# Kernel tuning notes

Measured on AMD Instinct MI355X. Metric: run time of the kernel, lower is better.

## Reference

```python
import jax, jax.numpy as jnp
import numpy as np

B, K, DIN, D, NH, HD, FF = 16384, 64, 49, 16, 2, 8, 32
EPS = 1e-5


def _ln(x, g, b):
    m = jnp.mean(x, axis=-1, keepdims=True)
    v = jnp.mean((x - m) ** 2, axis=-1, keepdims=True)
    return (x - m) / jnp.sqrt(v + EPS) * g + b


def setup_inputs() -> dict:
    key = jax.random.key(0)
    ks = jax.random.split(key, 20)
    s = 0.05
    return {
        "x": jax.random.normal(ks[0], (B, K, DIN), dtype=jnp.float32),
        # torch Linear layout: weight is [out, in]
        "proj_w": jax.random.normal(ks[1], (D, DIN), dtype=jnp.float32) * s,
        "proj_b": jax.random.normal(ks[2], (D,), dtype=jnp.float32) * s,
        "pos": jax.random.normal(ks[3], (1, K, D), dtype=jnp.float32) * s,
        "in_proj_w": jax.random.normal(ks[4], (3 * D, D), dtype=jnp.float32) * s,
        "in_proj_b": jax.random.normal(ks[5], (3 * D,), dtype=jnp.float32) * s,
        "out_w": jax.random.normal(ks[6], (D, D), dtype=jnp.float32) * s,
        "out_b": jax.random.normal(ks[7], (D,), dtype=jnp.float32) * s,
        "ln1_g": jnp.ones((D,), dtype=jnp.float32),
        "ln1_b": jnp.zeros((D,), dtype=jnp.float32),
        "lin1_w": jax.random.normal(ks[8], (FF, D), dtype=jnp.float32) * s,
        "lin1_b": jax.random.normal(ks[9], (FF,), dtype=jnp.float32) * s,
        "lin2_w": jax.random.normal(ks[10], (D, FF), dtype=jnp.float32) * s,
        "lin2_b": jax.random.normal(ks[11], (D,), dtype=jnp.float32) * s,
        "ln2_g": jnp.ones((D,), dtype=jnp.float32),
        "ln2_b": jnp.zeros((D,), dtype=jnp.float32),
        "head_w": jax.random.normal(ks[12], (1, D), dtype=jnp.float32) * s,
        "head_b": jax.random.normal(ks[13], (1,), dtype=jnp.float32) * s,
    }


def reference(x, proj_w, proj_b, pos, in_proj_w, in_proj_b, out_w, out_b,
              ln1_g, ln1_b, lin1_w, lin1_b, lin2_w, lin2_b, ln2_g, ln2_b,
              head_w, head_b):
    # input projection + learned positional embedding
    h = jnp.einsum("bki,di->bkd", x, proj_w) + proj_b + pos  # [B,K,D]

    # --- self-attention (torch MultiheadAttention, post-norm encoder layer) ---
    qkv = jnp.einsum("bkd,ed->bke", h, in_proj_w) + in_proj_b  # [B,K,3D]
    q, k, v = jnp.split(qkv, 3, axis=-1)
    q = q.reshape(B, K, NH, HD)
    k = k.reshape(B, K, NH, HD)
    v = v.reshape(B, K, NH, HD)
    scores = jnp.einsum("bqhd,bkhd->bhqk", q, k) / jnp.sqrt(jnp.float32(HD))
    attn = jax.nn.softmax(scores, axis=-1)
    ctx = jnp.einsum("bhqk,bkhd->bqhd", attn, v).reshape(B, K, D)
    attn_out = jnp.einsum("bkd,od->bko", ctx, out_w) + out_b
    h = _ln(h + attn_out, ln1_g, ln1_b)

    # --- FFN (relu), post-norm ---
    ff = jnp.einsum("bkd,fd->bkf", h, lin1_w) + lin1_b
    ff = jax.nn.relu(ff)
    ff = jnp.einsum("bkf,df->bkd", ff, lin2_w) + lin2_b
    h = _ln(h + ff, ln2_g, ln2_b)

    # mean pool over sequence, then scalar head
    pooled = h.mean(axis=1)  # [B,D]
    out = jnp.einsum("bd,od->bo", pooled, head_w) + head_b
    return out.squeeze(-1)  # [B]
```

## Files before the change

### kernel.cpp

```cpp
#include <hip/hip_runtime.h>


#define SCALE 0.510069729f

#define KRS   24
#define VTB   1536
#define VTS   72
#define HRB   2688
#define HRS   40
#define RED   5248
#define SMTOT 5256

#define WS_HB   2304
#define WS_EP   3328

typedef __bf16 v8bf __attribute__((ext_vector_type(8)));
typedef float  v4f  __attribute__((ext_vector_type(4)));

#define LDS_ORDER() __asm__ volatile("" ::: "memory")

static __device__ __forceinline__ short f2bs(float f) {
    __bf16 h = (__bf16)f;
    return __builtin_bit_cast(short, h);
}
#define MFMA(a,b,c) __builtin_amdgcn_mfma_f32_16x16x32_bf16((a),(b),(c),0,0,0)

template<int IMM> static __device__ __forceinline__ float swz(float x) {
    return __builtin_bit_cast(float,
        __builtin_amdgcn_ds_swizzle(__builtin_bit_cast(int, x), IMM));
}

template<int CTRL> static __device__ __forceinline__ float dppadd(float v) {
    int t = __builtin_amdgcn_update_dpp(0, __builtin_bit_cast(int, v),
                                        CTRL, 0xF, 0xF, true);
    return v + __builtin_bit_cast(float, t);
}

static __device__ __forceinline__ void red16(v4f& v) {
    #pragma unroll
    for (int r = 0; r < 4; ++r) v[r] = dppadd<0xB1>(v[r]);
    #pragma unroll
    for (int r = 0; r < 4; ++r) v[r] = dppadd<0x4E>(v[r]);
    #pragma unroll
    for (int r = 0; r < 4; ++r) v[r] = dppadd<0x124>(v[r]);
    #pragma unroll
    for (int r = 0; r < 4; ++r) v[r] = dppadd<0x128>(v[r]);
}

__global__ __launch_bounds__(256)
void tx_prep(const float* __restrict__ proj_w, const float* __restrict__ proj_b,
             const float* __restrict__ pos,
             const float* __restrict__ in_proj_w, const float* __restrict__ in_proj_b,
             const float* __restrict__ out_w, const float* __restrict__ out_b,
             const float* __restrict__ ln1_g, const float* __restrict__ ln1_b,
             const float* __restrict__ lin1_w, const float* __restrict__ lin1_b,
             const float* __restrict__ lin2_w, const float* __restrict__ lin2_b,
             const float* __restrict__ ln2_g, const float* __restrict__ ln2_b,
             const float* __restrict__ head_w, float* __restrict__ ws)
{
    const int tid = threadIdx.x;
    const int wv = tid >> 6, lane = tid & 63;
    const int g = lane >> 4, c = lane & 15;
    v8bf* wf = (v8bf*)ws;
    v8bf F;
    if (wv == 0) {
        #pragma unroll
        for (int j = 0; j < 8; ++j) F[j] = (__bf16)proj_w[c*49 + g*8 + j];
        wf[0*64 + lane] = F;
        #pragma unroll
        for (int j = 0; j < 8; ++j) {
            int k = (g == 0) ? (32 + j) : (g == 1) ? (40 + j)
                  : (g == 2 && j == 7) ? 48 : -1;
            F[j] = (k >= 0) ? (__bf16)proj_w[c*49 + k] : (__bf16)0.f;
        }
        wf[1*64 + lane] = F;
        #pragma unroll
        for (int nt = 0; nt < 3; ++nt) {
            #pragma unroll
            for (int j = 0; j < 8; ++j) { int k = g*8 + j; F[j] = (k < 16) ? (__bf16)in_proj_w[(nt*16 + c)*16 + k] : (__bf16)0.f; }
            wf[(2 + nt)*64 + lane] = F;
        }
    } else if (wv == 1) {
        #pragma unroll
        for (int j = 0; j < 8; ++j) { int k = g*8 + j; F[j] = (k < 16) ? (__bf16)out_w[c*16 + k] : (__bf16)0.f; }
        wf[5*64 + lane] = F;
        #pragma unroll
        for (int nt = 0; nt < 2; ++nt) {
            #pragma unroll
            for (int j = 0; j < 8; ++j) { int k = g*8 + j; F[j] = (k < 16) ? (__bf16)lin1_w[(nt*16 + c)*16 + k] : (__bf16)0.f; }
            wf[(6 + nt)*64 + lane] = F;
        }
        #pragma unroll
        for (int j = 0; j < 8; ++j) F[j] = (__bf16)lin2_w[c*32 + g*8 + j];
        wf[8*64 + lane] = F;
        if (lane < 16) {
            float* ep = ws + WS_EP + lane*16;
            ep[0]  = in_proj_b[lane];
            ep[1]  = in_proj_b[16 + lane] * SCALE;
            ep[2]  = in_proj_b[32 + lane];
            ep[3]  = out_b[lane];
            ep[4]  = ln1_g[lane];
            ep[5]  = ln1_b[lane];
            ep[6]  = lin1_b[lane];
            ep[7]  = lin1_b[16 + lane];
            ep[8]  = lin2_b[lane];
            ep[9]  = ln2_g[lane];
            ep[10] = ln2_b[lane];
            ep[11] = head_w[lane];
            ep[12] = 0.f; ep[13] = 0.f; ep[14] = 0.f; ep[15] = 0.f;
        }
    } else {
        float* hb = ws + WS_HB;
        const int w0 = (wv - 2) * 2;
        #pragma unroll
        for (int i = 0; i < 2; ++i) {
            int ww = w0 + i;
            #pragma unroll
            for (int r = 0; r < 4; ++r)
                hb[ww*256 + lane*4 + r] = proj_b[c] + pos[(ww*16 + g*4 + r)*16 + c];
        }
    }
}

__global__ __launch_bounds__(256, 8)
void tx_main(const float* __restrict__ x, const float* __restrict__ ws,
             const float* __restrict__ head_b, float* __restrict__ out)
{
    __shared__ __align__(16) short sm[SMTOT];
    const int tid   = threadIdx.x;
    const int w     = tid >> 6;
    const int lane  = tid & 63;
    const int g     = lane >> 4;
    const int c     = lane & 15;
    const int b     = blockIdx.x;
    const int myrow = w*16 + c;
    const int tok0  = w*16 + g*4;
    const v8bf* wf  = (const v8bf*)ws;
    const float4* ep4 = (const float4*)(ws + WS_EP);

    v8bf zfrag;
    #pragma unroll
    for (int j = 0; j < 8; ++j) zfrag[j] = (__bf16)0.f;
    const v4f zacc = {0.f, 0.f, 0.f, 0.f};

    *(unsigned long long*)&sm[HRB + myrow*HRS + 16 + g*4] = 0ull;
    if (lane < 16) {
        float4 z4 = {0.f, 0.f, 0.f, 0.f};
        *(float4*)&sm[(w*16 + lane)*KRS + 16] = z4;
    }

    v4f hC;
    {
        const float* xr = x + (size_t)b * 3136 + myrow*49;
        int off1 = 32 + g*8; if (off1 > 41) off1 = 41;
        v8bf a0, a1;
        #pragma unroll
        for (int j = 0; j < 8; ++j) a0[j] = (__bf16)xr[g*8 + j];
        #pragma unroll
        for (int j = 0; j < 8; ++j) a1[j] = (__bf16)xr[off1 + j];
        v4f hb = ((const v4f*)(ws + WS_HB))[w*64 + lane];
        hC = MFMA(a0, wf[0*64 + lane], hb);
        hC = MFMA(a1, wf[1*64 + lane], hC);
        #pragma unroll
        for (int r = 0; r < 4; ++r) sm[HRB + (tok0 + r)*HRS + c] = f2bs(hC[r]);
    }
    LDS_ORDER();

    {
        v8bf a = *(const v8bf*)&sm[HRB + myrow*HRS + g*8];
        v4f qC = MFMA(a, wf[2*64 + lane], zacc);
        v4f kC = MFMA(a, wf[3*64 + lane], zacc);
        v4f vC = MFMA(a, wf[4*64 + lane], zacc);
        float4 e0 = ep4[c*4];
        const int vsl = VTB + c*VTS + 32*(w >> 1) + 8*g + 4*(w & 1);
        #pragma unroll
        for (int r = 0; r < 4; ++r) {
            int tok = tok0 + r;
            sm[HRB + tok*HRS + c] = f2bs(qC[r] + e0.x);
            sm[tok*KRS + c]       = f2bs(fmaf(kC[r], SCALE, e0.y));
            sm[vsl + r]           = f2bs(vC[r] + e0.z);
        }
    }
    __syncthreads();

    v4f ctxC0, ctxC1;
    {
        v8bf aq = *(const v8bf*)&sm[HRB + myrow*HRS + g*8];
        #pragma unroll
        for (int hh = 0; hh < 2; ++hh) {
            v8bf bq = (g == hh) ? aq : zfrag;
            v8bf plo, phi;
            {
                v8bf ak0 = *(const v8bf*)&sm[(0*16 + c)*KRS + g*8];
                v8bf ak1 = *(const v8bf*)&sm[(1*16 + c)*KRS + g*8];
                v4f s0 = MFMA(ak0, bq, zacc);
                v4f s1 = MFMA(ak1, bq, zacc);
                #pragma unroll
                for (int r = 0; r < 4; ++r) {
                    plo[r]     = (__bf16)__builtin_amdgcn_exp2f(s0[r]);
                    plo[4 + r] = (__bf16)__builtin_amdgcn_exp2f(s1[r]);
                }
                v8bf ak2 = *(const v8bf*)&sm[(2*16 + c)*KRS + g*8];
                v8bf ak3 = *(const v8bf*)&sm[(3*16 + c)*KRS + g*8];
                v4f s2 = MFMA(ak2, bq, zacc);
                v4f s3 = MFMA(ak3, bq, zacc);
                #pragma unroll
                for (int r = 0; r < 4; ++r) {
                    phi[r]     = (__bf16)__builtin_amdgcn_exp2f(s2[r]);
                    phi[4 + r] = (__bf16)__builtin_amdgcn_exp2f(s3[r]);
                }
            }
            v8bf bv0 = zfrag, bv1 = zfrag;
            bool act  = (hh == 0) ? (c < 8) : (c >= 8);
            int  onec = (hh == 0) ? 8 : 7;
            if (act) {
                bv0 = *(const v8bf*)&sm[VTB + c*VTS + g*8];
                bv1 = *(const v8bf*)&sm[VTB + c*VTS + 32 + g*8];
            } else if (c == onec) {
                #pragma unroll
                for (int j = 0; j < 8; ++j) { bv0[j] = (__bf16)1.f; bv1[j] = (__bf16)1.f; }
            }
            v4f acc = MFMA(plo, bv0, zacc);
            acc = MFMA(phi, bv1, acc);
            if (hh) ctxC1 = acc; else ctxC0 = acc;
        }
    }

    {
        #pragma unroll
        for (int r = 0; r < 4; ++r) {
            float l0 = swz<0x110>(ctxC0[r]);
            float l1 = swz<0x0F0>(ctxC1[r]);
            float num = (c < 8) ? ctxC0[r] : ctxC1[r];
            float den = (c < 8) ? l0 : l1;
            sm[HRB + (tok0 + r)*HRS + c] = f2bs(num * __builtin_amdgcn_rcpf(den));
        }
    }
    LDS_ORDER();

    v4f hln;
    {
        v8bf a = *(const v8bf*)&sm[HRB + myrow*HRS + g*8];
        v4f oC = MFMA(a, wf[5*64 + lane], hC);
        float4 e0 = ep4[c*4];
        float4 e1 = ep4[c*4 + 1];
        v4f hn, s, q;
        #pragma unroll
        for (int r = 0; r < 4; ++r) { hn[r] = oC[r] + e0.w; s[r] = hn[r]; q[r] = hn[r]*hn[r]; }
        red16(s);
        red16(q);
        #pragma unroll
        for (int r = 0; r < 4; ++r) {
            float mean = s[r]*0.0625f;
            float is = __builtin_amdgcn_rsqf(fmaf(q[r], 0.0625f, fmaf(mean, -mean, 1e-5f)));
            hln[r] = (hn[r] - mean)*is*e1.x + e1.y;
            sm[HRB + (tok0 + r)*HRS + c] = f2bs(hln[r]);
        }
    }
    LDS_ORDER();

    v4f o2;
    {
        v8bf a = *(const v8bf*)&sm[HRB + myrow*HRS + g*8];
        v4f f0 = MFMA(a, wf[6*64 + lane], zacc);
        v4f f1 = MFMA(a, wf[7*64 + lane], zacc);
        float4 e1 = ep4[c*4 + 1];
        #pragma unroll
        for (int r = 0; r < 4; ++r) {
            int tok = tok0 + r;
            sm[HRB + tok*HRS + c]      = f2bs(fmaxf(f0[r] + e1.z, 0.f));
            sm[HRB + tok*HRS + 16 + c] = f2bs(fmaxf(f1[r] + e1.w, 0.f));
        }
        LDS_ORDER();
        v8bf a2 = *(const v8bf*)&sm[HRB + myrow*HRS + g*8];
        o2 = MFMA(a2, wf[8*64 + lane], hln);
    }

    float part = 0.f;
    {
        float4 e2 = ep4[c*4 + 2];
        v4f hn, s, q;
        #pragma unroll
        for (int r = 0; r < 4; ++r) { hn[r] = o2[r] + e2.x; s[r] = hn[r]; q[r] = hn[r]*hn[r]; }
        red16(s);
        red16(q);
        #pragma unroll
        for (int r = 0; r < 4; ++r) {
            float mean = s[r]*0.0625f;
            float is = __builtin_amdgcn_rsqf(fmaf(q[r], 0.0625f, fmaf(mean, -mean, 1e-5f)));
            float h3 = (hn[r] - mean)*is*e2.y + e2.z;
            part = fmaf(h3, e2.w, part);
        }
    }
    part = dppadd<0xB1>(part);
    part = dppadd<0x4E>(part);
    part = dppadd<0x124>(part);
    part = dppadd<0x128>(part);
    part += swz<0x401F>(part);
    part += __shfl_xor(part, 32, 64);
    float* fred = (float*)&sm[RED];
    if (lane == 0) fred[w] = part;
    __syncthreads();
    if (tid == 0)
        out[b] = (fred[0] + fred[1] + fred[2] + fred[3]) * (1.f/64.f) + head_b[0];
}

extern "C" void kernel_launch(void* const* d_in, const int* in_sizes, int n_in,
                              void* d_out, int out_size, void* d_ws, size_t ws_size,
                              hipStream_t stream) {
    const float* x         = (const float*)d_in[0];
    const float* proj_w    = (const float*)d_in[1];
    const float* proj_b    = (const float*)d_in[2];
    const float* pos       = (const float*)d_in[3];
    const float* in_proj_w = (const float*)d_in[4];
    const float* in_proj_b = (const float*)d_in[5];
    const float* out_w     = (const float*)d_in[6];
    const float* out_b     = (const float*)d_in[7];
    const float* ln1_g     = (const float*)d_in[8];
    const float* ln1_b     = (const float*)d_in[9];
    const float* lin1_w    = (const float*)d_in[10];
    const float* lin1_b    = (const float*)d_in[11];
    const float* lin2_w    = (const float*)d_in[12];
    const float* lin2_b    = (const float*)d_in[13];
    const float* ln2_g     = (const float*)d_in[14];
    const float* ln2_b     = (const float*)d_in[15];
    const float* head_w    = (const float*)d_in[16];
    const float* head_b    = (const float*)d_in[17];
    float* ws = (float*)d_ws;

    tx_prep<<<1, 256, 0, stream>>>(proj_w, proj_b, pos, in_proj_w, in_proj_b,
                                   out_w, out_b, ln1_g, ln1_b, lin1_w, lin1_b,
                                   lin2_w, lin2_b, ln2_g, ln2_b, head_w, ws);
    tx_main<<<16384, 256, 0, stream>>>(x, ws, head_b, (float*)d_out);
}
```

Measured before the change: 318.1 us.

## Process two batch samples per block with interleaved MFMA chains

Each block now handles two batch elements instead of one, doubling the shared memory buffers and interleaving independent MFMA chains for both samples. This halves the grid, amortises weight-fragment loads and the per-block barrier and reduction overhead, and adds instruction-level parallelism to hide MFMA and LDS latency. In exchange it uses more registers and LDS per block and lowers the occupancy target from 8 to 6 blocks.

```diff
diff --git a/kernel.cpp b/kernel.cpp
--- a/kernel.cpp
+++ b/kernel.cpp
@@ -9,7 +9,8 @@
 #define HRB   2688
 #define HRS   40
 #define RED   5248
-#define SMTOT 5256
+#define HALF  5256
+#define SMTOT 10512
 
 #define WS_HB   2304
 #define WS_EP   3328
@@ -122,7 +123,7 @@
     }
 }
 
-__global__ __launch_bounds__(256, 8)
+__global__ __launch_bounds__(256, 6)
 void tx_main(const float* __restrict__ x, const float* __restrict__ ws,
              const float* __restrict__ head_b, float* __restrict__ out)
 {
@@ -132,7 +133,7 @@
     const int lane  = tid & 63;
     const int g     = lane >> 4;
     const int c     = lane & 15;
-    const int b     = blockIdx.x;
+    const int b0    = blockIdx.x * 2;
     const int myrow = w*16 + c;
     const int tok0  = w*16 + g*4;
     const v8bf* wf  = (const v8bf*)ws;
@@ -144,165 +145,239 @@
     const v4f zacc = {0.f, 0.f, 0.f, 0.f};
 
     *(unsigned long long*)&sm[HRB + myrow*HRS + 16 + g*4] = 0ull;
+    *(unsigned long long*)&sm[HALF + HRB + myrow*HRS + 16 + g*4] = 0ull;
     if (lane < 16) {
         float4 z4 = {0.f, 0.f, 0.f, 0.f};
         *(float4*)&sm[(w*16 + lane)*KRS + 16] = z4;
-    }
-
-    v4f hC;
-    {
-        const float* xr = x + (size_t)b * 3136 + myrow*49;
+        *(float4*)&sm[HALF + (w*16 + lane)*KRS + 16] = z4;
+    }
+
+    v4f hC0, hC1;
+    {
+        const float* xr0 = x + (size_t)b0 * 3136 + myrow*49;
+        const float* xr1 = xr0 + 3136;
         int off1 = 32 + g*8; if (off1 > 41) off1 = 41;
-        v8bf a0, a1;
-        #pragma unroll
-        for (int j = 0; j < 8; ++j) a0[j] = (__bf16)xr[g*8 + j];
-        #pragma unroll
-        for (int j = 0; j < 8; ++j) a1[j] = (__bf16)xr[off1 + j];
+        v8bf a00, a01, a10, a11;
+        #pragma unroll
+        for (int j = 0; j < 8; ++j) a00[j] = (__bf16)xr0[g*8 + j];
+        #pragma unroll
+        for (int j = 0; j < 8; ++j) a01[j] = (__bf16)xr0[off1 + j];
+        #pragma unroll
+        for (int j = 0; j < 8; ++j) a10[j] = (__bf16)xr1[g*8 + j];
+        #pragma unroll
+        for (int j = 0; j < 8; ++j) a11[j] = (__bf16)xr1[off1 + j];
         v4f hb = ((const v4f*)(ws + WS_HB))[w*64 + lane];
-        hC = MFMA(a0, wf[0*64 + lane], hb);
-        hC = MFMA(a1, wf[1*64 + lane], hC);
-        #pragma unroll
-        for (int r = 0; r < 4; ++r) sm[HRB + (tok0 + r)*HRS + c] = f2bs(hC[r]);
+        v8bf Bp0 = wf[0*64 + lane], Bp1 = wf[1*64 + lane];
+        hC0 = MFMA(a00, Bp0, hb);
+        hC1 = MFMA(a10, Bp0, hb);
+        hC0 = MFMA(a01, Bp1, hC0);
+        hC1 = MFMA(a11, Bp1, hC1);
+        #pragma unroll
+        for (int r = 0; r < 4; ++r) {
+            sm[HRB + (tok0 + r)*HRS + c]        = f2bs(hC0[r]);
+            sm[HALF + HRB + (tok0 + r)*HRS + c] = f2bs(hC1[r]);
+        }
     }
     LDS_ORDER();
 
     {
-        v8bf a = *(const v8bf*)&sm[HRB + myrow*HRS + g*8];
-        v4f qC = MFMA(a, wf[2*64 + lane], zacc);
-        v4f kC = MFMA(a, wf[3*64 + lane], zacc);
-        v4f vC = MFMA(a, wf[4*64 + lane], zacc);
+        v8bf aA = *(const v8bf*)&sm[HRB + myrow*HRS + g*8];
+        v8bf aB = *(const v8bf*)&sm[HALF + HRB + myrow*HRS + g*8];
+        v8bf Bq0 = wf[2*64 + lane], Bq1 = wf[3*64 + lane], Bq2 = wf[4*64 + lane];
+        v4f qC0 = MFMA(aA, Bq0, zacc);
+        v4f qC1 = MFMA(aB, Bq0, zacc);
+        v4f kC0 = MFMA(aA, Bq1, zacc);
+        v4f kC1 = MFMA(aB, Bq1, zacc);
+        v4f vC0 = MFMA(aA, Bq2, zacc);
+        v4f vC1 = MFMA(aB, Bq2, zacc);
         float4 e0 = ep4[c*4];
         const int vsl = VTB + c*VTS + 32*(w >> 1) + 8*g + 4*(w & 1);
         #pragma unroll
         for (int r = 0; r < 4; ++r) {
             int tok = tok0 + r;
-            sm[HRB + tok*HRS + c] = f2bs(qC[r] + e0.x);
-            sm[tok*KRS + c]       = f2bs(fmaf(kC[r], SCALE, e0.y));
-            sm[vsl + r]           = f2bs(vC[r] + e0.z);
+            sm[HRB + tok*HRS + c]        = f2bs(qC0[r] + e0.x);
+            sm[HALF + HRB + tok*HRS + c] = f2bs(qC1[r] + e0.x);
+            sm[tok*KRS + c]              = f2bs(fmaf(kC0[r], SCALE, e0.y));
+            sm[HALF + tok*KRS + c]       = f2bs(fmaf(kC1[r], SCALE, e0.y));
+            sm[vsl + r]                  = f2bs(vC0[r] + e0.z);
+            sm[HALF + vsl + r]           = f2bs(vC1[r] + e0.z);
         }
     }
     __syncthreads();
 
-    v4f ctxC0, ctxC1;
-    {
-        v8bf aq = *(const v8bf*)&sm[HRB + myrow*HRS + g*8];
+    v4f ctx00, ctx01, ctx10, ctx11;
+    {
+        v8bf aq0 = *(const v8bf*)&sm[HRB + myrow*HRS + g*8];
+        v8bf aq1 = *(const v8bf*)&sm[HALF + HRB + myrow*HRS + g*8];
         #pragma unroll
         for (int hh = 0; hh < 2; ++hh) {
-            v8bf bq = (g == hh) ? aq : zfrag;
-            v8bf plo, phi;
+            v8bf bq0 = (g == hh) ? aq0 : zfrag;
+            v8bf bq1 = (g == hh) ? aq1 : zfrag;
+            v8bf plo0, phi0, plo1, phi1;
             {
-                v8bf ak0 = *(const v8bf*)&sm[(0*16 + c)*KRS + g*8];
-                v8bf ak1 = *(const v8bf*)&sm[(1*16 + c)*KRS + g*8];
-                v4f s0 = MFMA(ak0, bq, zacc);
-                v4f s1 = MFMA(ak1, bq, zacc);
+                v8bf k0 = *(const v8bf*)&sm[(0*16 + c)*KRS + g*8];
+                v8bf k1 = *(const v8bf*)&sm[(1*16 + c)*KRS + g*8];
+                v8bf k2 = *(const v8bf*)&sm[(2*16 + c)*KRS + g*8];
+                v8bf k3 = *(const v8bf*)&sm[(3*16 + c)*KRS + g*8];
+                v4f s0 = MFMA(k0, bq0, zacc);
+                v4f s1 = MFMA(k1, bq0, zacc);
+                v4f s2 = MFMA(k2, bq0, zacc);
+                v4f s3 = MFMA(k3, bq0, zacc);
                 #pragma unroll
                 for (int r = 0; r < 4; ++r) {
-                    plo[r]     = (__bf16)__builtin_amdgcn_exp2f(s0[r]);
-                    plo[4 + r] = (__bf16)__builtin_amdgcn_exp2f(s1[r]);
+                    plo0[r]     = (__bf16)__builtin_amdgcn_exp2f(s0[r]);
+                    plo0[4 + r] = (__bf16)__builtin_amdgcn_exp2f(s1[r]);
+                    phi0[r]     = (__bf16)__builtin_amdgcn_exp2f(s2[r]);
+                    phi0[4 + r] = (__bf16)__builtin_amdgcn_exp2f(s3[r]);
                 }
-                v8bf ak2 = *(const v8bf*)&sm[(2*16 + c)*KRS + g*8];
-                v8bf ak3 = *(const v8bf*)&sm[(3*16 + c)*KRS + g*8];
-                v4f s2 = MFMA(ak2, bq, zacc);
-                v4f s3 = MFMA(ak3, bq, zacc);
+                v8bf m0 = *(const v8bf*)&sm[HALF + (0*16 + c)*KRS + g*8];
+                v8bf m1 = *(const v8bf*)&sm[HALF + (1*16 + c)*KRS + g*8];
+                v8bf m2 = *(const v8bf*)&sm[HALF + (2*16 + c)*KRS + g*8];
+                v8bf m3 = *(const v8bf*)&sm[HALF + (3*16 + c)*KRS + g*8];
+                v4f t0 = MFMA(m0, bq1, zacc);
+                v4f t1 = MFMA(m1, bq1, zacc);
+                v4f t2 = MFMA(m2, bq1, zacc);
+                v4f t3 = MFMA(m3, bq1, zacc);
                 #pragma unroll
                 for (int r = 0; r < 4; ++r) {
-                    phi[r]     = (__bf16)__builtin_amdgcn_exp2f(s2[r]);
-                    phi[4 + r] = (__bf16)__builtin_amdgcn_exp2f(s3[r]);
+                    plo1[r]     = (__bf16)__builtin_amdgcn_exp2f(t0[r]);
+                    plo1[4 + r] = (__bf16)__builtin_amdgcn_exp2f(t1[r]);
+                    phi1[r]     = (__bf16)__builtin_amdgcn_exp2f(t2[r]);
+                    phi1[4 + r] = (__bf16)__builtin_amdgcn_exp2f(t3[r]);
                 }
             }
-            v8bf bv0 = zfrag, bv1 = zfrag;
+            v8bf bv00 = zfrag, bv10 = zfrag, bv01 = zfrag, bv11 = zfrag;
             bool act  = (hh == 0) ? (c < 8) : (c >= 8);
             int  onec = (hh == 0) ? 8 : 7;
             if (act) {
-                bv0 = *(const v8bf*)&sm[VTB + c*VTS + g*8];
-                bv1 = *(const v8bf*)&sm[VTB + c*VTS + 32 + g*8];
+                bv00 = *(const v8bf*)&sm[VTB + c*VTS + g*8];
+                bv10 = *(const v8bf*)&sm[VTB + c*VTS + 32 + g*8];
+                bv01 = *(const v8bf*)&sm[HALF + VTB + c*VTS + g*8];
+                bv11 = *(const v8bf*)&sm[HALF + VTB + c*VTS + 32 + g*8];
             } else if (c == onec) {
                 #pragma unroll
-                for (int j = 0; j < 8; ++j) { bv0[j] = (__bf16)1.f; bv1[j] = (__bf16)1.f; }
+                for (int j = 0; j < 8; ++j) {
+                    bv00[j] = (__bf16)1.f; bv10[j] = (__bf16)1.f;
+                    bv01[j] = (__bf16)1.f; bv11[j] = (__bf16)1.f;
+                }
             }
-            v4f acc = MFMA(plo, bv0, zacc);
-            acc = MFMA(phi, bv1, acc);
-            if (hh) ctxC1 = acc; else ctxC0 = acc;
-        }
-    }
-
-    {
-        #pragma unroll
-        for (int r = 0; r < 4; ++r) {
-            float l0 = swz<0x110>(ctxC0[r]);
-            float l1 = swz<0x0F0>(ctxC1[r]);
-            float num = (c < 8) ? ctxC0[r] : ctxC1[r];
-            float den = (c < 8) ? l0 : l1;
-            sm[HRB + (tok0 + r)*HRS + c] = f2bs(num * __builtin_amdgcn_rcpf(den));
+            v4f a0 = MFMA(plo0, bv00, zacc);
+            a0 = MFMA(phi0, bv10, a0);
+            v4f a1 = MFMA(plo1, bv01, zacc);
+            a1 = MFMA(phi1, bv11, a1);
+            if (hh) { ctx01 = a0; ctx11 = a1; }
+            else    { ctx00 = a0; ctx10 = a1; }
+        }
+    }
+
+    {
+        #pragma unroll
+        for (int r = 0; r < 4; ++r) {
+            float l00 = swz<0x110>(ctx00[r]);
+            float l01 = swz<0x0F0>(ctx01[r]);
+            float l10 = swz<0x110>(ctx10[r]);
+            float l11 = swz<0x0F0>(ctx11[r]);
+            float n0 = (c < 8) ? ctx00[r] : ctx01[r];
+            float d0 = (c < 8) ? l00 : l01;
+            float n1 = (c < 8) ? ctx10[r] : ctx11[r];
+            float d1 = (c < 8) ? l10 : l11;
+            sm[HRB + (tok0 + r)*HRS + c]        = f2bs(n0 * __builtin_amdgcn_rcpf(d0));
+            sm[HALF + HRB + (tok0 + r)*HRS + c] = f2bs(n1 * __builtin_amdgcn_rcpf(d1));
         }
     }
     LDS_ORDER();
 
-    v4f hln;
-    {
-        v8bf a = *(const v8bf*)&sm[HRB + myrow*HRS + g*8];
-        v4f oC = MFMA(a, wf[5*64 + lane], hC);
+    v4f hln0, hln1;
+    {
+        v8bf aA = *(const v8bf*)&sm[HRB + myrow*HRS + g*8];
+        v8bf aB = *(const v8bf*)&sm[HALF + HRB + myrow*HRS + g*8];
+        v8bf Bo = wf[5*64 + lane];
+        v4f oC0 = MFMA(aA, Bo, hC0);
+        v4f oC1 = MFMA(aB, Bo, hC1);
         float4 e0 = ep4[c*4];
         float4 e1 = ep4[c*4 + 1];
-        v4f hn, s, q;
-        #pragma unroll
-        for (int r = 0; r < 4; ++r) { hn[r] = oC[r] + e0.w; s[r] = hn[r]; q[r] = hn[r]*hn[r]; }
-        red16(s);
-        red16(q);
-        #pragma unroll
-        for (int r = 0; r < 4; ++r) {
-            float mean = s[r]*0.0625f;
-            float is = __builtin_amdgcn_rsqf(fmaf(q[r], 0.0625f, fmaf(mean, -mean, 1e-5f)));
-            hln[r] = (hn[r] - mean)*is*e1.x + e1.y;
-            sm[HRB + (tok0 + r)*HRS + c] = f2bs(hln[r]);
+        v4f hn0, s0, q0, hn1, s1, q1;
+        #pragma unroll
+        for (int r = 0; r < 4; ++r) {
+            hn0[r] = oC0[r] + e0.w; s0[r] = hn0[r]; q0[r] = hn0[r]*hn0[r];
+            hn1[r] = oC1[r] + e0.w; s1[r] = hn1[r]; q1[r] = hn1[r]*hn1[r];
+        }
+        red16(s0); red16(q0); red16(s1); red16(q1);
+        #pragma unroll
+        for (int r = 0; r < 4; ++r) {
+            float m0 = s0[r]*0.0625f;
+            float i0 = __builtin_amdgcn_rsqf(fmaf(q0[r], 0.0625f, fmaf(m0, -m0, 1e-5f)));
+            hln0[r] = (hn0[r] - m0)*i0*e1.x + e1.y;
+            sm[HRB + (tok0 + r)*HRS + c] = f2bs(hln0[r]);
+            float m1 = s1[r]*0.0625f;
+            float i1 = __builtin_amdgcn_rsqf(fmaf(q1[r], 0.0625f, fmaf(m1, -m1, 1e-5f)));
+            hln1[r] = (hn1[r] - m1)*i1*e1.x + e1.y;
+            sm[HALF + HRB + (tok0 + r)*HRS + c] = f2bs(hln1[r]);
         }
     }
     LDS_ORDER();
 
-    v4f o2;
-    {
-        v8bf a = *(const v8bf*)&sm[HRB + myrow*HRS + g*8];
-        v4f f0 = MFMA(a, wf[6*64 + lane], zacc);
-        v4f f1 = MFMA(a, wf[7*64 + lane], zacc);
+    v4f o20, o21;
+    {
+        v8bf aA = *(const v8bf*)&sm[HRB + myrow*HRS + g*8];
+        v8bf aB = *(const v8bf*)&sm[HALF + HRB + myrow*HRS + g*8];
+        v8bf Bl10 = wf[6*64 + lane], Bl11 = wf[7*64 + lane];
+        v4f f00 = MFMA(aA, Bl10, zacc);
+        v4f f01 = MFMA(aA, Bl11, zacc);
+        v4f f10 = MFMA(aB, Bl10, zacc);
+        v4f f11 = MFMA(aB, Bl11, zacc);
         float4 e1 = ep4[c*4 + 1];
         #pragma unroll
         for (int r = 0; r < 4; ++r) {
             int tok = tok0 + r;
-            sm[HRB + tok*HRS + c]      = f2bs(fmaxf(f0[r] + e1.z, 0.f));
-            sm[HRB + tok*HRS + 16 + c] = f2bs(fmaxf(f1[r] + e1.w, 0.f));
+            sm[HRB + tok*HRS + c]             = f2bs(fmaxf(f00[r] + e1.z, 0.f));
+            sm[HRB + tok*HRS + 16 + c]        = f2bs(fmaxf(f01[r] + e1.w, 0.f));
+            sm[HALF + HRB + tok*HRS + c]      = f2bs(fmaxf(f10[r] + e1.z, 0.f));
+            sm[HALF + HRB + tok*HRS + 16 + c] = f2bs(fmaxf(f11[r] + e1.w, 0.f));
         }
         LDS_ORDER();
-        v8bf a2 = *(const v8bf*)&sm[HRB + myrow*HRS + g*8];
-        o2 = MFMA(a2, wf[8*64 + lane], hln);
-    }
-
-    float part = 0.f;
+        v8bf Bl2 = wf[8*64 + lane];
+        v8bf a2A = *(const v8bf*)&sm[HRB + myrow*HRS + g*8];
+        v8bf a2B = *(const v8bf*)&sm[HALF + HRB + myrow*HRS + g*8];
+        o20 = MFMA(a2A, Bl2, hln0);
+        o21 = MFMA(a2B, Bl2, hln1);
+    }
+
+    float part0 = 0.f, part1 = 0.f;
     {
         float4 e2 = ep4[c*4 + 2];
-        v4f hn, s, q;
-        #pragma unroll
-        for (int r = 0; r < 4; ++r) { hn[r] = o2[r] + e2.x; s[r] = hn[r]; q[r] = hn[r]*hn[r]; }
-        red16(s);
-        red16(q);
-        #pragma unroll
-        for (int r = 0; r < 4; ++r) {
-            float mean = s[r]*0.0625f;
-            float is = __builtin_amdgcn_rsqf(fmaf(q[r], 0.0625f, fmaf(mean, -mean, 1e-5f)));
-            float h3 = (hn[r] - mean)*is*e2.y + e2.z;
-            part = fmaf(h3, e2.w, part);
-        }
-    }
-    part = dppadd<0xB1>(part);
-    part = dppadd<0x4E>(part);
-    part = dppadd<0x124>(part);
-    part = dppadd<0x128>(part);
-    part += swz<0x401F>(part);
-    part += __shfl_xor(part, 32, 64);
-    float* fred = (float*)&sm[RED];
-    if (lane == 0) fred[w] = part;
+        v4f hn0, s0, q0, hn1, s1, q1;
+        #pragma unroll
+        for (int r = 0; r < 4; ++r) {
+            hn0[r] = o20[r] + e2.x; s0[r] = hn0[r]; q0[r] = hn0[r]*hn0[r];
+            hn1[r] = o21[r] + e2.x; s1[r] = hn1[r]; q1[r] = hn1[r]*hn1[r];
+        }
+        red16(s0); red16(q0); red16(s1); red16(q1);
+        #pragma unroll
+        for (int r = 0; r < 4; ++r) {
+            float m0 = s0[r]*0.0625f;
+            float i0 = __builtin_amdgcn_rsqf(fmaf(q0[r], 0.0625f, fmaf(m0, -m0, 1e-5f)));
+            part0 = fmaf((hn0[r] - m0)*i0*e2.y + e2.z, e2.w, part0);
+            float m1 = s1[r]*0.0625f;
+            float i1 = __builtin_amdgcn_rsqf(fmaf(q1[r], 0.0625f, fmaf(m1, -m1, 1e-5f)));
+            part1 = fmaf((hn1[r] - m1)*i1*e2.y + e2.z, e2.w, part1);
+        }
+    }
+    part0 = dppadd<0xB1>(part0);  part1 = dppadd<0xB1>(part1);
+    part0 = dppadd<0x4E>(part0);  part1 = dppadd<0x4E>(part1);
+    part0 = dppadd<0x124>(part0); part1 = dppadd<0x124>(part1);
+    part0 = dppadd<0x128>(part0); part1 = dppadd<0x128>(part1);
+    part0 += swz<0x401F>(part0);  part1 += swz<0x401F>(part1);
+    part0 += __shfl_xor(part0, 32, 64);
+    part1 += __shfl_xor(part1, 32, 64);
+    float* fr0 = (float*)&sm[RED];
+    float* fr1 = (float*)&sm[HALF + RED];
+    if (lane == 0) { fr0[w] = part0; fr1[w] = part1; }
     __syncthreads();
-    if (tid == 0)
-        out[b] = (fred[0] + fred[1] + fred[2] + fred[3]) * (1.f/64.f) + head_b[0];
+    if (tid < 2) {
+        const float* fr = (tid == 0) ? fr0 : fr1;
+        out[b0 + tid] = (fr[0] + fr[1] + fr[2] + fr[3]) * (1.f/64.f) + head_b[0];
+    }
 }
 
 extern "C" void kernel_launch(void* const* d_in, const int* in_sizes, int n_in,
@@ -331,5 +406,5 @@
     tx_prep<<<1, 256, 0, stream>>>(proj_w, proj_b, pos, in_proj_w, in_proj_b,
                                    out_w, out_b, ln1_g, ln1_b, lin1_w, lin1_b,
                                    lin2_w, lin2_b, ln2_g, ln2_b, head_w, ws);
-    tx_main<<<16384, 256, 0, stream>>>(x, ws, head_b, (float*)d_out);
-}
+    tx_main<<<8192, 256, 0, stream>>>(x, ws, head_b, (float*)d_out);
+}
```

Result: slower. 381.9 us (+20.1%).
